# Kernel optimization log

Hardware: AMD Instinct MI355X
Metric: run time of the kernel (lower is better)

Reference implementation:

```python
import jax, jax.numpy as jnp
import numpy as np

MARGIN = 0.3
EPS = 1e-12


def setup_inputs() -> dict:
    key = jax.random.key(0)
    k1, k2 = jax.random.split(key)
    inputs = jax.random.normal(k1, (256, 2048), dtype=jnp.float32)
    targets = jax.random.randint(k2, (256,), 0, 32, dtype=jnp.int64)
    return {"inputs": inputs, "targets": targets}


def reference(inputs, targets):
    # Pairwise Euclidean distance matrix [n, n] via GEMM.
    sq = jnp.sum(inputs * inputs, axis=1)                      # [n]
    dist = sq[:, None] + sq[None, :] - 2.0 * (inputs @ inputs.T)
    dist = jnp.sqrt(jnp.clip(dist, EPS, None))                 # [n, n]

    same = targets[:, None] == targets[None, :]                # [n, n]
    # Triplet margin for all (anchor, positive, negative) in one broadcast.
    tri = dist[:, :, None] - dist[:, None, :] + MARGIN         # [n, n, n]
    tri = jnp.clip(tri, EPS, None)
    # Valid: same label for (a, p), different label for (a, neg).
    valid = same[:, :, None] & (~same)[:, None, :]             # [n, n, n]
    # Torch version stacks only valid triplets (dynamic shape); here we
    # return the dense [n, n, n] tensor with invalid entries zeroed.
    return jnp.where(valid, tri, 0.0)
```

## Files before the change

### kernel.cpp

```cpp
#include <hip/hip_runtime.h>
#include <hip/hip_fp16.h>

#define N 256
#define D 2048
#define MARGIN_F 0.3f
#define EPS_F 1e-12f
#define SQRT_EPS_F 1e-6f

typedef float v4f __attribute__((ext_vector_type(4)));

__global__ __launch_bounds__(64) void sq_kernel(const float* __restrict__ x,
                                                float* __restrict__ sq) {
    int row = blockIdx.x;
    int lane = threadIdx.x;
    const float4* xr = (const float4*)(x + (size_t)row * D);
    float acc = 0.f;
#pragma unroll
    for (int it = 0; it < 8; ++it) {
        float4 v = xr[lane + 64 * it];
        acc += v.x * v.x + v.y * v.y + v.z * v.z + v.w * v.w;
    }
#pragma unroll
    for (int off = 32; off > 0; off >>= 1) acc += __shfl_down(acc, off, 64);
    if (lane == 0) sq[row] = acc;
}

__global__ __launch_bounds__(256) void gram_kernel(const float* __restrict__ x,
                                                   __half* __restrict__ part) {
    __shared__ __align__(16) float As[64 * 68];
    __shared__ __align__(16) float Bs[64 * 68];
    const int i0 = blockIdx.x * 64, j0 = blockIdx.y * 64, k0 = blockIdx.z * 64;
    const int tid = threadIdx.x;

#pragma unroll
    for (int it = 0; it < 4; ++it) {
        int f = tid + 256 * it;
        int row = f >> 4;
        int c4 = f & 15;
        int sc4 = c4 ^ ((row >> 2) & 15);
        float4 va = *(const float4*)(x + (size_t)(i0 + row) * D + k0 + c4 * 4);
        float4 vb = *(const float4*)(x + (size_t)(j0 + row) * D + k0 + c4 * 4);
        *(float4*)(As + row * 68 + sc4 * 4) = va;
        *(float4*)(Bs + row * 68 + sc4 * 4) = vb;
    }
    __syncthreads();

    const int tx = tid & 15;
    const int ty = tid >> 4;
    float acc[4][4];
#pragma unroll
    for (int r = 0; r < 4; ++r)
#pragma unroll
        for (int c = 0; c < 4; ++c) acc[r][c] = 0.f;

#pragma unroll
    for (int k4 = 0; k4 < 16; ++k4) {
        float4 a[4], b[4];
        const int ca = (k4 ^ ty) << 2;
        const int cb = (k4 ^ tx) << 2;
#pragma unroll
        for (int r = 0; r < 4; ++r) {
            a[r] = *(const float4*)(As + (ty * 4 + r) * 68 + ca);
            b[r] = *(const float4*)(Bs + (tx * 4 + r) * 68 + cb);
        }
#pragma unroll
        for (int r = 0; r < 4; ++r)
#pragma unroll
            for (int c = 0; c < 4; ++c)
                acc[r][c] += a[r].x * b[c].x + a[r].y * b[c].y +
                             a[r].z * b[c].z + a[r].w * b[c].w;
    }

    __half* pout = part + (size_t)blockIdx.z * (N * N);
#pragma unroll
    for (int r = 0; r < 4; ++r) {
        int gi = i0 + ty * 4 + r;
        union { __half2 h2[2]; uint2 u; } pk;
        pk.h2[0] = __floats2half2_rn(acc[r][0], acc[r][1]);
        pk.h2[1] = __floats2half2_rn(acc[r][2], acc[r][3]);
        *(uint2*)(pout + (size_t)gi * N + j0 + tx * 4) = pk.u;
    }
}

__global__ __launch_bounds__(256) void fused_kernel(const __half* __restrict__ part,
                                                    const float* __restrict__ sq,
                                                    const int* __restrict__ targets,
                                                    float* __restrict__ out) {
    __shared__ __align__(16) float drow[N];
    __shared__ int lab[N];
    const int a = blockIdx.x;
    const int tid = threadIdx.x;
    lab[tid] = targets[tid];

    float dot = 0.f;
    const __half* base = part + a * N + tid;
#pragma unroll 8
    for (int ks = 0; ks < 32; ++ks)
        dot += __half2float(base[(size_t)ks * (N * N)]);
    drow[tid] = (tid == a) ? SQRT_EPS_F
                           : sqrtf(fmaxf(sq[a] + sq[tid] - 2.f * dot, EPS_F));
    __syncthreads();

    const int la = lab[a];
    const int lane = tid & 63;
    const int pq = tid >> 6;
    const int p0 = blockIdx.y * 128 + pq * 32;

    v4f dan = *(const v4f*)(drow + lane * 4);
    v4f mb = MARGIN_F - dan;
    v4f nokv = {(lab[lane * 4 + 0] != la) ? 1.f : 0.f,
                (lab[lane * 4 + 1] != la) ? 1.f : 0.f,
                (lab[lane * 4 + 2] != la) ? 1.f : 0.f,
                (lab[lane * 4 + 3] != la) ? 1.f : 0.f};

    float* obase = out + ((size_t)a << 16) + lane * 4;
#pragma unroll 4
    for (int i = 0; i < 32; ++i) {
        int p = p0 + i;
        v4f r = {0.f, 0.f, 0.f, 0.f};
        if (lab[p] == la) {
            float dap = drow[p];
            v4f t = dap + mb;
            t.x = fmaxf(t.x, EPS_F);
            t.y = fmaxf(t.y, EPS_F);
            t.z = fmaxf(t.z, EPS_F);
            t.w = fmaxf(t.w, EPS_F);
            r = t * nokv;
        }
        __builtin_nontemporal_store(r, (v4f*)(obase + (size_t)p * N));
    }
}

__global__ __launch_bounds__(256) void dist_kernel(const __half* __restrict__ part,
                                                   const float* __restrict__ sq,
                                                   float* __restrict__ dist) {
    const int a = blockIdx.x;
    const int tid = threadIdx.x;
    float dot = 0.f;
    const __half* base = part + a * N + tid;
#pragma unroll 8
    for (int ks = 0; ks < 32; ++ks)
        dot += __half2float(base[(size_t)ks * (N * N)]);
    dist[a * N + tid] = (tid == a) ? SQRT_EPS_F
                                   : sqrtf(fmaxf(sq[a] + sq[tid] - 2.f * dot, EPS_F));
}

__global__ __launch_bounds__(256) void triplet_kernel(const float* __restrict__ dist,
                                                      const int* __restrict__ targets,
                                                      float* __restrict__ out) {
    __shared__ __align__(16) float drow[N];
    __shared__ int lab[N];
    const int a = blockIdx.x;
    const int p0 = blockIdx.y * 16;
    const int tid = threadIdx.x;
    lab[tid] = targets[tid];
    drow[tid] = dist[a * N + tid];
    __syncthreads();

    const int la = lab[a];
    const int lane = tid & 63;
    const int pq = tid >> 6;

    v4f dan = *(const v4f*)(drow + lane * 4);
    v4f mb = MARGIN_F - dan;
    v4f nokv = {(lab[lane * 4 + 0] != la) ? 1.f : 0.f,
                (lab[lane * 4 + 1] != la) ? 1.f : 0.f,
                (lab[lane * 4 + 2] != la) ? 1.f : 0.f,
                (lab[lane * 4 + 3] != la) ? 1.f : 0.f};

    float* obase = out + ((size_t)a << 16) + lane * 4;
#pragma unroll
    for (int j = 0; j < 4; ++j) {
        int p = p0 + pq * 4 + j;
        v4f r = {0.f, 0.f, 0.f, 0.f};
        if (lab[p] == la) {
            float dap = drow[p];
            v4f t = dap + mb;
            t.x = fmaxf(t.x, EPS_F);
            t.y = fmaxf(t.y, EPS_F);
            t.z = fmaxf(t.z, EPS_F);
            t.w = fmaxf(t.w, EPS_F);
            r = t * nokv;
        }
        __builtin_nontemporal_store(r, (v4f*)(obase + (size_t)p * N));
    }
}

extern "C" void kernel_launch(void* const* d_in, const int* in_sizes, int n_in,
                              void* d_out, int out_size, void* d_ws, size_t ws_size,
                              hipStream_t stream) {
    const float* x = (const float*)d_in[0];
    const int* targets = (const int*)d_in[1];
    float* out = (float*)d_out;
    float* ws = (float*)d_ws;

    float* sq = ws;
    size_t need_full = 1024 + (size_t)32 * N * N * sizeof(__half) + 1024;

    if (ws_size >= need_full) {
        __half* part = (__half*)(ws + 256);
        sq_kernel<<<256, 64, 0, stream>>>(x, sq);
        gram_kernel<<<dim3(4, 4, 32), 256, 0, stream>>>(x, part);
        fused_kernel<<<dim3(256, 2), 256, 0, stream>>>(part, sq, targets, out);
    } else {
        __half* part = (__half*)d_out;
        float* dist = ws + 256;
        sq_kernel<<<256, 64, 0, stream>>>(x, sq);
        gram_kernel<<<dim3(4, 4, 32), 256, 0, stream>>>(x, part);
        dist_kernel<<<256, 256, 0, stream>>>(part, sq, dist);
        triplet_kernel<<<dim3(256, 16), 256, 0, stream>>>(dist, targets, out);
    }
}
```

Baseline: 92.46 us.

## Compute Gram matrix with bf16 MFMA and fewer K-slices, fuse bf16 conversion

Adds a kernel that converts inputs to bf16 while computing squared norms. The Gram matrix is then computed with MFMA 16x16x32 bf16 instructions over 8 K-slices, with fp32 partials laid out per row, replacing the LDS-tiled VALU GEMM with 32 fp16 partials. This cuts GEMM compute time and partial-sum traffic, at the cost of bf16 input precision. The output stores switch from nontemporal to regular stores.

```diff
diff --git a/kernel.cpp b/kernel.cpp
--- a/kernel.cpp
+++ b/kernel.cpp
@@ -6,83 +6,65 @@
 #define MARGIN_F 0.3f
 #define EPS_F 1e-12f
 #define SQRT_EPS_F 1e-6f
+#define KSLICES 8
 
 typedef float v4f __attribute__((ext_vector_type(4)));
-
-__global__ __launch_bounds__(64) void sq_kernel(const float* __restrict__ x,
-                                                float* __restrict__ sq) {
-    int row = blockIdx.x;
-    int lane = threadIdx.x;
-    const float4* xr = (const float4*)(x + (size_t)row * D);
-    float acc = 0.f;
-#pragma unroll
-    for (int it = 0; it < 8; ++it) {
-        float4 v = xr[lane + 64 * it];
-        acc += v.x * v.x + v.y * v.y + v.z * v.z + v.w * v.w;
-    }
+typedef short bf16x8 __attribute__((ext_vector_type(8)));
+
+static __device__ __forceinline__ unsigned short f2bf_rne(float f) {
+    union { float f; unsigned u; } v; v.f = f;
+    unsigned r = v.u + 0x7fffu + ((v.u >> 16) & 1u);
+    return (unsigned short)(r >> 16);
+}
+
+__global__ __launch_bounds__(256) void conv_sq_kernel(const float* __restrict__ x,
+                                                      unsigned short* __restrict__ xb,
+                                                      float* __restrict__ sq) {
+    __shared__ float red[4];
+    const int row = blockIdx.x;
+    const int tid = threadIdx.x;
+    const float* xr = x + (size_t)row * D + tid * 8;
+    float4 v0 = *(const float4*)(xr);
+    float4 v1 = *(const float4*)(xr + 4);
+    float acc = v0.x * v0.x + v0.y * v0.y + v0.z * v0.z + v0.w * v0.w +
+                v1.x * v1.x + v1.y * v1.y + v1.z * v1.z + v1.w * v1.w;
+    union { unsigned short h[8]; uint4 u; } pk;
+    pk.h[0] = f2bf_rne(v0.x); pk.h[1] = f2bf_rne(v0.y);
+    pk.h[2] = f2bf_rne(v0.z); pk.h[3] = f2bf_rne(v0.w);
+    pk.h[4] = f2bf_rne(v1.x); pk.h[5] = f2bf_rne(v1.y);
+    pk.h[6] = f2bf_rne(v1.z); pk.h[7] = f2bf_rne(v1.w);
+    *(uint4*)(xb + (size_t)row * D + tid * 8) = pk.u;
 #pragma unroll
     for (int off = 32; off > 0; off >>= 1) acc += __shfl_down(acc, off, 64);
-    if (lane == 0) sq[row] = acc;
-}
-
-__global__ __launch_bounds__(256) void gram_kernel(const float* __restrict__ x,
-                                                   __half* __restrict__ part) {
-    __shared__ __align__(16) float As[64 * 68];
-    __shared__ __align__(16) float Bs[64 * 68];
-    const int i0 = blockIdx.x * 64, j0 = blockIdx.y * 64, k0 = blockIdx.z * 64;
-    const int tid = threadIdx.x;
-
-#pragma unroll
-    for (int it = 0; it < 4; ++it) {
-        int f = tid + 256 * it;
-        int row = f >> 4;
-        int c4 = f & 15;
-        int sc4 = c4 ^ ((row >> 2) & 15);
-        float4 va = *(const float4*)(x + (size_t)(i0 + row) * D + k0 + c4 * 4);
-        float4 vb = *(const float4*)(x + (size_t)(j0 + row) * D + k0 + c4 * 4);
-        *(float4*)(As + row * 68 + sc4 * 4) = va;
-        *(float4*)(Bs + row * 68 + sc4 * 4) = vb;
-    }
-    __syncthreads();
-
-    const int tx = tid & 15;
-    const int ty = tid >> 4;
-    float acc[4][4];
+    if ((tid & 63) == 0) red[tid >> 6] = acc;
+    __syncthreads();
+    if (tid == 0) sq[row] = red[0] + red[1] + red[2] + red[3];
+}
+
+__global__ __launch_bounds__(256) void gram_mfma_kernel(const unsigned short* __restrict__ xb,
+                                                        float* __restrict__ part) {
+    const int w = threadIdx.x >> 6;
+    const int l = threadIdx.x & 63;
+    const int i0 = blockIdx.x * 32 + (w >> 1) * 16;
+    const int j0 = blockIdx.y * 32 + (w & 1) * 16;
+    const int ks = blockIdx.z;
+    const int kq = (l >> 4) * 8;
+    const unsigned short* pa = xb + (size_t)(i0 + (l & 15)) * D + ks * 256 + kq;
+    const unsigned short* pb = xb + (size_t)(j0 + (l & 15)) * D + ks * 256 + kq;
+    v4f acc = {0.f, 0.f, 0.f, 0.f};
+#pragma unroll
+    for (int t = 0; t < 8; ++t) {
+        bf16x8 af = *(const bf16x8*)(pa + t * 32);
+        bf16x8 bf = *(const bf16x8*)(pb + t * 32);
+        acc = __builtin_amdgcn_mfma_f32_16x16x32_bf16(af, bf, acc, 0, 0, 0);
+    }
+    float* pp = part + ((size_t)(i0 + (l >> 4) * 4) * KSLICES + ks) * N + j0 + (l & 15);
 #pragma unroll
     for (int r = 0; r < 4; ++r)
-#pragma unroll
-        for (int c = 0; c < 4; ++c) acc[r][c] = 0.f;
-
-#pragma unroll
-    for (int k4 = 0; k4 < 16; ++k4) {
-        float4 a[4], b[4];
-        const int ca = (k4 ^ ty) << 2;
-        const int cb = (k4 ^ tx) << 2;
-#pragma unroll
-        for (int r = 0; r < 4; ++r) {
-            a[r] = *(const float4*)(As + (ty * 4 + r) * 68 + ca);
-            b[r] = *(const float4*)(Bs + (tx * 4 + r) * 68 + cb);
-        }
-#pragma unroll
-        for (int r = 0; r < 4; ++r)
-#pragma unroll
-            for (int c = 0; c < 4; ++c)
-                acc[r][c] += a[r].x * b[c].x + a[r].y * b[c].y +
-                             a[r].z * b[c].z + a[r].w * b[c].w;
-    }
-
-    __half* pout = part + (size_t)blockIdx.z * (N * N);
-#pragma unroll
-    for (int r = 0; r < 4; ++r) {
-        int gi = i0 + ty * 4 + r;
-        union { __half2 h2[2]; uint2 u; } pk;
-        pk.h2[0] = __floats2half2_rn(acc[r][0], acc[r][1]);
-        pk.h2[1] = __floats2half2_rn(acc[r][2], acc[r][3]);
-        *(uint2*)(pout + (size_t)gi * N + j0 + tx * 4) = pk.u;
-    }
-}
-
-__global__ __launch_bounds__(256) void fused_kernel(const __half* __restrict__ part,
+        pp[(size_t)r * KSLICES * N] = acc[r];
+}
+
+__global__ __launch_bounds__(256) void fused_kernel(const float* __restrict__ part,
                                                     const float* __restrict__ sq,
                                                     const int* __restrict__ targets,
                                                     float* __restrict__ out) {
@@ -92,11 +74,11 @@
     const int tid = threadIdx.x;
     lab[tid] = targets[tid];
 
+    const float* pr = part + (size_t)a * (KSLICES * N);
     float dot = 0.f;
-    const __half* base = part + a * N + tid;
-#pragma unroll 8
-    for (int ks = 0; ks < 32; ++ks)
-        dot += __half2float(base[(size_t)ks * (N * N)]);
+#pragma unroll
+    for (int ks = 0; ks < KSLICES; ++ks)
+        dot += pr[ks * N + tid];
     drow[tid] = (tid == a) ? SQRT_EPS_F
                            : sqrtf(fmaxf(sq[a] + sq[tid] - 2.f * dot, EPS_F));
     __syncthreads();
@@ -127,7 +109,74 @@
             t.w = fmaxf(t.w, EPS_F);
             r = t * nokv;
         }
-        __builtin_nontemporal_store(r, (v4f*)(obase + (size_t)p * N));
+        *(v4f*)(obase + (size_t)p * N) = r;
+    }
+}
+
+__global__ __launch_bounds__(64) void sq_kernel(const float* __restrict__ x,
+                                                float* __restrict__ sq) {
+    int row = blockIdx.x;
+    int lane = threadIdx.x;
+    const float4* xr = (const float4*)(x + (size_t)row * D);
+    float acc = 0.f;
+#pragma unroll
+    for (int it = 0; it < 8; ++it) {
+        float4 v = xr[lane + 64 * it];
+        acc += v.x * v.x + v.y * v.y + v.z * v.z + v.w * v.w;
+    }
+#pragma unroll
+    for (int off = 32; off > 0; off >>= 1) acc += __shfl_down(acc, off, 64);
+    if (lane == 0) sq[row] = acc;
+}
+
+__global__ __launch_bounds__(256) void gram_valu_kernel(const float* __restrict__ x,
+                                                        __half* __restrict__ part) {
+    __shared__ __align__(16) float As[64 * 68];
+    __shared__ __align__(16) float Bs[64 * 68];
+    const int i0 = blockIdx.x * 64, j0 = blockIdx.y * 64, k0 = blockIdx.z * 64;
+    const int tid = threadIdx.x;
+#pragma unroll
+    for (int it = 0; it < 4; ++it) {
+        int f = tid + 256 * it;
+        int row = f >> 4;
+        int c4 = f & 15;
+        int sc4 = c4 ^ ((row >> 2) & 15);
+        float4 va = *(const float4*)(x + (size_t)(i0 + row) * D + k0 + c4 * 4);
+        float4 vb = *(const float4*)(x + (size_t)(j0 + row) * D + k0 + c4 * 4);
+        *(float4*)(As + row * 68 + sc4 * 4) = va;
+        *(float4*)(Bs + row * 68 + sc4 * 4) = vb;
+    }
+    __syncthreads();
+    const int tx = tid & 15, ty = tid >> 4;
+    float acc[4][4];
+#pragma unroll
+    for (int r = 0; r < 4; ++r)
+#pragma unroll
+        for (int c = 0; c < 4; ++c) acc[r][c] = 0.f;
+#pragma unroll
+    for (int k4 = 0; k4 < 16; ++k4) {
+        float4 a[4], b[4];
+        const int ca = (k4 ^ ty) << 2, cb = (k4 ^ tx) << 2;
+#pragma unroll
+        for (int r = 0; r < 4; ++r) {
+            a[r] = *(const float4*)(As + (ty * 4 + r) * 68 + ca);
+            b[r] = *(const float4*)(Bs + (tx * 4 + r) * 68 + cb);
+        }
+#pragma unroll
+        for (int r = 0; r < 4; ++r)
+#pragma unroll
+            for (int c = 0; c < 4; ++c)
+                acc[r][c] += a[r].x * b[c].x + a[r].y * b[c].y +
+                             a[r].z * b[c].z + a[r].w * b[c].w;
+    }
+    __half* pout = part + (size_t)blockIdx.z * (N * N);
+#pragma unroll
+    for (int r = 0; r < 4; ++r) {
+        int gi = i0 + ty * 4 + r;
+        union { __half2 h2[2]; uint2 u; } pk;
+        pk.h2[0] = __floats2half2_rn(acc[r][0], acc[r][1]);
+        pk.h2[1] = __floats2half2_rn(acc[r][2], acc[r][3]);
+        *(uint2*)(pout + (size_t)gi * N + j0 + tx * 4) = pk.u;
     }
 }
 
@@ -156,18 +205,15 @@
     lab[tid] = targets[tid];
     drow[tid] = dist[a * N + tid];
     __syncthreads();
-
     const int la = lab[a];
     const int lane = tid & 63;
     const int pq = tid >> 6;
-
     v4f dan = *(const v4f*)(drow + lane * 4);
     v4f mb = MARGIN_F - dan;
     v4f nokv = {(lab[lane * 4 + 0] != la) ? 1.f : 0.f,
                 (lab[lane * 4 + 1] != la) ? 1.f : 0.f,
                 (lab[lane * 4 + 2] != la) ? 1.f : 0.f,
                 (lab[lane * 4 + 3] != la) ? 1.f : 0.f};
-
     float* obase = out + ((size_t)a << 16) + lane * 4;
 #pragma unroll
     for (int j = 0; j < 4; ++j) {
@@ -182,7 +228,7 @@
             t.w = fmaxf(t.w, EPS_F);
             r = t * nokv;
         }
-        __builtin_nontemporal_store(r, (v4f*)(obase + (size_t)p * N));
+        *(v4f*)(obase + (size_t)p * N) = r;
     }
 }
 
@@ -195,19 +241,20 @@
     float* ws = (float*)d_ws;
 
     float* sq = ws;
-    size_t need_full = 1024 + (size_t)32 * N * N * sizeof(__half) + 1024;
-
-    if (ws_size >= need_full) {
-        __half* part = (__half*)(ws + 256);
-        sq_kernel<<<256, 64, 0, stream>>>(x, sq);
-        gram_kernel<<<dim3(4, 4, 32), 256, 0, stream>>>(x, part);
+    unsigned short* xb = (unsigned short*)(ws + 256);
+    float* part = (float*)(xb + (size_t)N * D);
+    size_t need = 256 * 4 + (size_t)N * D * 2 + (size_t)KSLICES * N * N * 4 + 1024;
+
+    if (ws_size >= need) {
+        conv_sq_kernel<<<256, 256, 0, stream>>>(x, xb, sq);
+        gram_mfma_kernel<<<dim3(8, 8, 8), 256, 0, stream>>>(xb, part);
         fused_kernel<<<dim3(256, 2), 256, 0, stream>>>(part, sq, targets, out);
     } else {
-        __half* part = (__half*)d_out;
+        __half* hpart = (__half*)d_out;
         float* dist = ws + 256;
         sq_kernel<<<256, 64, 0, stream>>>(x, sq);
-        gram_kernel<<<dim3(4, 4, 32), 256, 0, stream>>>(x, part);
-        dist_kernel<<<256, 256, 0, stream>>>(part, sq, dist);
+        gram_valu_kernel<<<dim3(4, 4, 32), 256, 0, stream>>>(x, hpart);
+        dist_kernel<<<256, 256, 0, stream>>>(hpart, sq, dist);
         triplet_kernel<<<dim3(256, 16), 256, 0, stream>>>(dist, targets, out);
     }
 }
```

After: 84.81 us. 8.3% less time.
